# Kernel optimization log

Measured on AMD Instinct MI355X. Metric: run time of the kernel, lower is better.

The kernel has to match this reference:

```python
import jax, jax.numpy as jnp
import numpy as np

B, S, D = 2, 2048, 2560
H, HD = 32, 80           # n_head, head_dim = n_embd // n_head
RD = 32                  # rotary_dim (partial rotary, phi-style)
ROPE_BASE = 10000.0


def _rope_cache(seqlen, rotary_dim):
    # inv_freq = 1 / base^(2i/d); freqs = outer(t, inv_freq)  -> [S, RD//2]
    inv_freq = 1.0 / (ROPE_BASE ** (jnp.arange(0, rotary_dim, 2, dtype=jnp.float32) / rotary_dim))
    t = jnp.arange(seqlen, dtype=jnp.float32)
    freqs = jnp.outer(t, inv_freq)
    return jnp.cos(freqs), jnp.sin(freqs)


def setup_inputs() -> dict:
    key = jax.random.key(0)
    k0, k1, k2, k3, k4 = jax.random.split(key, 5)
    x = jax.random.normal(k0, (B, S, D), dtype=jnp.float32)
    wqkv_w = jax.random.normal(k1, (3 * D, D), dtype=jnp.float32) * 0.02
    wqkv_b = jax.random.normal(k2, (3 * D,), dtype=jnp.float32) * 0.02
    out_w = jax.random.normal(k3, (D, D), dtype=jnp.float32) * 0.02
    out_b = jax.random.normal(k4, (D,), dtype=jnp.float32) * 0.02
    return {"x": x, "wqkv_w": wqkv_w, "wqkv_b": wqkv_b, "out_w": out_w, "out_b": out_b}


def _attention_core(x, wqkv_w, wqkv_b, out_w, out_b):
    b, s, d = x.shape
    qkv = (x @ wqkv_w.T + wqkv_b).reshape(b, s, 3, H, HD)  # [B,S,3,H,HD]

    cos, sin = _rope_cache(s, RD)            # [S, RD//2]
    c = cos[:, None, :]                       # [S,1,RD//2]
    si = sin[:, None, :]

    def rot(t):  # partial NeoX-style rotary on first RD dims; t: [B,S,H,HD]
        t_rot, t_pass = t[..., :RD], t[..., RD:]
        t1, t2 = t_rot[..., : RD // 2], t_rot[..., RD // 2 :]
        return jnp.concatenate([t1 * c - t2 * si, t1 * si + t2 * c, t_pass], axis=-1)

    q = rot(qkv[:, :, 0])                     # [B,S,H,HD]
    k = rot(qkv[:, :, 1])
    v = qkv[:, :, 2]

    # fp32 scores = q @ (k * scale)^T, causal mask filled with -10000.0 (as in source)
    scale = 1.0 / np.sqrt(HD).astype(np.float32)
    scores = jnp.einsum("bqhd,bkhd->bhqk", q, k * scale)  # [B,H,S,S]
    causal_mask = jnp.arange(s)[None, :] > jnp.arange(s)[:, None]  # cols > rows
    scores = jnp.where(causal_mask, jnp.float32(-10000.0), scores)
    attn = jax.nn.softmax(scores, axis=-1)
    ctx = jnp.einsum("bhqk,bkhd->bqhd", attn, v).reshape(b, s, d)
    return ctx @ out_w.T + out_b


def reference(x, wqkv_w, wqkv_b, out_w, out_b):
    return _attention_core(x, wqkv_w, wqkv_b, out_w, out_b)
```

## Files before the change

### kernel.cpp

```cpp
#include <hip/hip_runtime.h>
#include <cstdint>
#include <cstddef>

#define B_  2
#define S_  2048
#define D_  2560
#define H_  32
#define HD_ 80

typedef __attribute__((ext_vector_type(8))) short  short8;
typedef __attribute__((ext_vector_type(4))) float  floatx4;

__device__ __forceinline__ float b2f(unsigned short u) {
  union { unsigned int i; float f; } x; x.i = ((unsigned int)u) << 16; return x.f;
}
__device__ __forceinline__ unsigned short f2bf(float f) {
  union { float f; unsigned int i; } x; x.f = f;
  unsigned int u = x.i;
  return (unsigned short)((u + 0x7fffu + ((u >> 16) & 1u)) >> 16);
}

__global__ void cvt3_kernel(const float* __restrict__ s0, unsigned short* __restrict__ d0, int n0,
                            const float* __restrict__ s1, unsigned short* __restrict__ d1, int n1,
                            const float* __restrict__ s2, unsigned short* __restrict__ d2, int n2) {
  int j = blockIdx.x * 256 + threadIdx.x;
  const float* s; unsigned short* d;
  if (j < n0) { s = s0; d = d0; }
  else {
    j -= n0;
    if (j < n1) { s = s1; d = d1; }
    else { j -= n1; if (j >= n2) return; s = s2; d = d2; }
  }
  const float4 v = ((const float4*)s)[j];
  ushort4 r;
  r.x = f2bf(v.x); r.y = f2bf(v.y); r.z = f2bf(v.z); r.w = f2bf(v.w);
  ((ushort4*)d)[j] = r;
}

#define GLOAD_LDS16(g, l)                                                      \
  __builtin_amdgcn_global_load_lds(                                            \
      (const __attribute__((address_space(1))) void*)(g),                      \
      (__attribute__((address_space(3))) void*)(l), 16, 0, 0)

template <int OUT_BF16>
__global__ __launch_bounds__(512)
void gemm256(const unsigned short* __restrict__ A,
             const unsigned short* __restrict__ Bw,
             const float* __restrict__ bias,
             void* __restrict__ Cv,
             const int M, const int N, const int K) {
  __shared__ __align__(16) unsigned short sh[65536];
  const int tid  = threadIdx.x;
  const int wave = tid >> 6;
  const int lane = tid & 63;
  const int wm = wave >> 2;
  const int wn = wave & 3;
  const int fr = lane & 15;
  const int fg = lane >> 4;
  const int row0 = (int)blockIdx.y << 8;
  const int col0 = (int)blockIdx.x << 8;
  const unsigned short* Ab = A  + (size_t)row0 * K;
  const unsigned short* Bb = Bw + (size_t)col0 * K;
  const int srow = lane >> 2;
  const int scol = ((lane & 3) << 3) ^ ((lane & 32) ? 16 : 0);
  const int rdoff = fr * 32 + ((fg * 8) ^ ((fr & 8) ? 16 : 0));
  const int aOff = wm * 8192;
  const int bOff = 16384 + (wn >> 1) * 8192;
  const int rbB  = (wn & 1) * 4;
  const int NT = K >> 6;

  floatx4 acc[8][4] = {};

#define STAGE_HALF(G, matOff, c, h, k0)                                        \
  do {                                                                         \
    _Pragma("unroll")                                                          \
    for (int i_ = 0; i_ < 2; ++i_) {                                           \
      const int s_ = (wave << 1) | i_;                                         \
      const int kk_ = s_ >> 3, rb_ = s_ & 7;                                   \
      GLOAD_LDS16((G) + (size_t)((h) * 128 + rb_ * 16 + srow) * K              \
                      + ((k0) + kk_ * 32 + scol),                              \
                  &sh[(c) * 32768 + (matOff) + (h) * 8192 + s_ * 512]);        \
    }                                                                          \
  } while (0)

  STAGE_HALF(Ab, 0,     0, 0, 0);
  STAGE_HALF(Ab, 0,     0, 1, 0);
  STAGE_HALF(Bb, 16384, 0, 0, 0);
  STAGE_HALF(Bb, 16384, 0, 1, 0);
  if (NT > 1) { STAGE_HALF(Ab, 0, 1, 0, 64); STAGE_HALF(Ab, 0, 1, 1, 64); }
  if (NT > 1) asm volatile("s_waitcnt vmcnt(4)" ::: "memory");
  else        asm volatile("s_waitcnt vmcnt(0)" ::: "memory");
  __builtin_amdgcn_s_barrier();

  for (int t = 0; t < NT; ++t) {
    const int c  = t & 1;
    const int cb = c << 15;
    short8 aF[4][2], bF0[2][2], bF1[2][2];
#pragma unroll
    for (int nj = 0; nj < 2; ++nj)
#pragma unroll
      for (int kk = 0; kk < 2; ++kk)
        bF0[nj][kk] = *(const short8*)&sh[cb + bOff + (kk * 8 + rbB + nj) * 512 + rdoff];
#pragma unroll
    for (int mi = 0; mi < 4; ++mi)
#pragma unroll
      for (int kk = 0; kk < 2; ++kk)
        aF[mi][kk] = *(const short8*)&sh[cb + aOff + (kk * 8 + mi) * 512 + rdoff];
    if (t + 1 < NT) STAGE_HALF(Bb, 16384, c ^ 1, 0, (t + 1) << 6);
    __builtin_amdgcn_s_barrier();
    __builtin_amdgcn_s_setprio(1);
#pragma unroll
    for (int kk = 0; kk < 2; ++kk)
#pragma unroll
      for (int mi = 0; mi < 4; ++mi)
#pragma unroll
        for (int nj = 0; nj < 2; ++nj)
          acc[mi][nj] = __builtin_amdgcn_mfma_f32_16x16x32_bf16(aF[mi][kk], bF0[nj][kk], acc[mi][nj], 0, 0, 0);
    __builtin_amdgcn_s_setprio(0);
    __builtin_amdgcn_s_barrier();
#pragma unroll
    for (int nj = 0; nj < 2; ++nj)
#pragma unroll
      for (int kk = 0; kk < 2; ++kk)
        bF1[nj][kk] = *(const short8*)&sh[cb + bOff + (kk * 8 + rbB + 2 + nj) * 512 + rdoff];
    if (t + 1 < NT) STAGE_HALF(Bb, 16384, c ^ 1, 1, (t + 1) << 6);
    __builtin_amdgcn_s_barrier();
    __builtin_amdgcn_s_setprio(1);
#pragma unroll
    for (int kk = 0; kk < 2; ++kk)
#pragma unroll
      for (int mi = 0; mi < 4; ++mi)
#pragma unroll
        for (int nj = 0; nj < 2; ++nj)
          acc[mi][2 + nj] = __builtin_amdgcn_mfma_f32_16x16x32_bf16(aF[mi][kk], bF1[nj][kk], acc[mi][2 + nj], 0, 0, 0);
    __builtin_amdgcn_s_setprio(0);
    __builtin_amdgcn_s_barrier();
#pragma unroll
    for (int mi = 0; mi < 4; ++mi)
#pragma unroll
      for (int kk = 0; kk < 2; ++kk)
        aF[mi][kk] = *(const short8*)&sh[cb + aOff + (kk * 8 + 4 + mi) * 512 + rdoff];
    __builtin_amdgcn_s_barrier();
    __builtin_amdgcn_s_setprio(1);
#pragma unroll
    for (int kk = 0; kk < 2; ++kk)
#pragma unroll
      for (int mi = 0; mi < 4; ++mi)
#pragma unroll
        for (int nj = 0; nj < 2; ++nj)
          acc[4 + mi][2 + nj] = __builtin_amdgcn_mfma_f32_16x16x32_bf16(aF[mi][kk], bF1[nj][kk], acc[4 + mi][2 + nj], 0, 0, 0);
    __builtin_amdgcn_s_setprio(0);
    __builtin_amdgcn_s_barrier();
    if (t + 2 < NT) {
      STAGE_HALF(Ab, 0, c, 0, (t + 2) << 6);
      STAGE_HALF(Ab, 0, c, 1, (t + 2) << 6);
    }
    __builtin_amdgcn_s_barrier();
    __builtin_amdgcn_s_setprio(1);
#pragma unroll
    for (int kk = 0; kk < 2; ++kk)
#pragma unroll
      for (int mi = 0; mi < 4; ++mi)
#pragma unroll
        for (int nj = 0; nj < 2; ++nj)
          acc[4 + mi][nj] = __builtin_amdgcn_mfma_f32_16x16x32_bf16(aF[mi][kk], bF0[nj][kk], acc[4 + mi][nj], 0, 0, 0);
    __builtin_amdgcn_s_setprio(0);
    if (t + 2 < NT)      asm volatile("s_waitcnt vmcnt(4)" ::: "memory");
    else if (t + 1 < NT) asm volatile("s_waitcnt vmcnt(0)" ::: "memory");
    __builtin_amdgcn_s_barrier();
  }
#undef STAGE_HALF

  unsigned short* Cb = (unsigned short*)Cv;
  float* Cf = (float*)Cv;
#pragma unroll
  for (int nj = 0; nj < 4; ++nj) {
    const int col = col0 + wn * 64 + nj * 16 + fr;
    const float bv = bias[col];
#pragma unroll
    for (int mi = 0; mi < 8; ++mi) {
      const int rowb = row0 + wm * 128 + mi * 16 + fg * 4;
#pragma unroll
      for (int r = 0; r < 4; ++r) {
        const float v = acc[mi][nj][r] + bv;
        const size_t idx = (size_t)(rowb + r) * N + col;
        if (OUT_BF16) Cb[idx] = f2bf(v);
        else          Cf[idx] = v;
      }
    }
  }
}

__global__ void rope_kernel(const unsigned short* __restrict__ qkv,
                            unsigned short* __restrict__ Q,
                            unsigned short* __restrict__ K) {
  const int idx = blockIdx.x * 256 + threadIdx.x;
  if (idx >= B_ * S_ * H_) return;
  const int h = idx & (H_ - 1);
  const int s = (idx >> 5) & (S_ - 1);
  const int b = idx >> 16;
  const unsigned short* row = qkv + (size_t)(b * S_ + s) * (3 * D_);
  const size_t obase = ((size_t)(b * H_ + h) * S_ + s) * HD_;

  float cc[16], ssn[16];
#pragma unroll
  for (int i = 0; i < 16; i++) {
    const float ang = (float)s * exp2f((float)i * -0.83048202372184059f);
    ssn[i] = sinf(ang);
    cc[i]  = cosf(ang);
  }
  {
    const float QS = 0.11180339887498949f * 1.4426950408889634f;
    const uint4* src = (const uint4*)(row + h * HD_);
    float f[80], g[80];
#pragma unroll
    for (int i = 0; i < 10; i++) {
      uint4 t = src[i];
      const unsigned short* w = (const unsigned short*)&t;
#pragma unroll
      for (int j = 0; j < 8; j++) f[i * 8 + j] = b2f(w[j]);
    }
#pragma unroll
    for (int i = 0; i < 16; i++) {
      g[i]      = f[i] * cc[i] - f[i + 16] * ssn[i];
      g[i + 16] = f[i] * ssn[i] + f[i + 16] * cc[i];
    }
#pragma unroll
    for (int i = 32; i < 80; i++) g[i] = f[i];
    uint4* dst = (uint4*)(Q + obase);
#pragma unroll
    for (int i = 0; i < 10; i++) {
      uint4 t;
      unsigned short* w = (unsigned short*)&t;
#pragma unroll
      for (int j = 0; j < 8; j++) w[j] = f2bf(g[i * 8 + j] * QS);
      dst[i] = t;
    }
  }
  {
    const uint4* src = (const uint4*)(row + (H_ + h) * HD_);
    float f[32], g[32];
#pragma unroll
    for (int i = 0; i < 4; i++) {
      uint4 t = src[i];
      const unsigned short* w = (const unsigned short*)&t;
#pragma unroll
      for (int j = 0; j < 8; j++) f[i * 8 + j] = b2f(w[j]);
    }
#pragma unroll
    for (int i = 0; i < 16; i++) {
      g[i]      = f[i] * cc[i] - f[i + 16] * ssn[i];
      g[i + 16] = f[i] * ssn[i] + f[i + 16] * cc[i];
    }
    uint4* dst = (uint4*)(K + obase);
#pragma unroll
    for (int i = 0; i < 4; i++) {
      uint4 t;
      unsigned short* w = (unsigned short*)&t;
#pragma unroll
      for (int j = 0; j < 8; j++) w[j] = f2bf(g[i * 8 + j]);
      dst[i] = t;
    }
#pragma unroll
    for (int i = 4; i < 10; i++) dst[i] = src[i];
  }
}

__global__ __launch_bounds__(256)
void vtrans_kernel(const unsigned short* __restrict__ qkv, unsigned short* __restrict__ Vt) {
  __shared__ unsigned short T[64][88];
  const int tid = threadIdx.x;
  const int bh = blockIdx.y;
  const int b = bh >> 5, h = bh & 31;
  const int tile = blockIdx.x;
  const int s0 = tile * 64;
  for (int t = tid; t < 640; t += 256) {
    const int r = t / 10, c = t % 10;
    const size_t src = ((size_t)((b * S_ + s0 + r) * 3) + 2) * D_ + h * HD_ + c * 8;
    *(uint4*)&T[r][c * 8] = *(const uint4*)&qkv[src];
  }
  __syncthreads();
  unsigned short* tb = Vt + ((size_t)bh * 32 + tile) * 5120;
  for (int t = tid; t < 640; t += 256) {
    const int d = t / 8, sc = t % 8;
    uint4 o;
    unsigned short* w = (unsigned short*)&o;
#pragma unroll
    for (int j = 0; j < 8; j++) w[j] = T[sc * 8 + j][d];
    *(uint4*)&tb[d * 64 + ((sc * 8) ^ ((d & 7) * 8))] = o;
  }
}

__global__ __launch_bounds__(256, 4)
void attn_mfma(const unsigned short* __restrict__ Qg,
               const unsigned short* __restrict__ Kg,
               const unsigned short* __restrict__ Vtg,
               unsigned short* __restrict__ ctx) {
  __shared__ unsigned short Ks[64 * 80];
  __shared__ unsigned short Vs[80 * 64];
  __shared__ unsigned short Ts[4][32 * 40];

  const int tid  = threadIdx.x;
  const int wave = tid >> 6;
  const int lane = tid & 63;
  const int fr   = lane & 15;
  const int fg   = lane >> 4;
  const int bh   = blockIdx.y;
  const int qt   = (int)gridDim.x - 1 - (int)blockIdx.x;
  const int qbase = (qt << 7) + wave * 32;

  const unsigned short* Qrow  = Qg  + (size_t)bh * S_ * HD_;
  const unsigned short* Krow  = Kg  + (size_t)bh * S_ * HD_;
  const unsigned short* Vtile = Vtg + (size_t)bh * 32 * 5120;

  short8 qf[2][3];
  const short8 zfrag = {};
#pragma unroll
  for (int mi = 0; mi < 2; mi++) {
    const unsigned short* qp = Qrow + (size_t)(qbase + mi * 16 + fr) * HD_;
    qf[mi][0] = *(const short8*)&qp[fg * 8];
    qf[mi][1] = *(const short8*)&qp[32 + fg * 8];
    qf[mi][2] = (fg < 2) ? *(const short8*)&qp[64 + fg * 8] : zfrag;
  }

  floatx4 accOT[5][2] = {};
  float l_part[2] = {0.f, 0.f};

  const int nch = 2 * qt + 2;
  for (int c = 0; c < nch; c++) {
    const int k0 = c * 64;
    __syncthreads();
    {
      const unsigned short* Kt = Krow + (size_t)k0 * HD_;
      for (int i = wave; i < 10; i += 4)
        GLOAD_LDS16(Kt + i * 512 + lane * 8, &Ks[i * 512]);
    }
    {
      const unsigned short* Vt = Vtile + (size_t)c * 5120;
      for (int i = wave; i < 10; i += 4)
        GLOAD_LDS16(Vt + i * 512 + lane * 8, &Vs[i * 512]);
    }
    __syncthreads();

    floatx4 accST[4][2] = {};
#pragma unroll
    for (int ni = 0; ni < 4; ni++) {
      const unsigned short* kp = &Ks[(ni * 16 + fr) * 80];
      const short8 kf0 = *(const short8*)&kp[fg * 8];
      const short8 kf1 = *(const short8*)&kp[32 + fg * 8];
      const short8 kf2 = *(const short8*)&kp[64 + (fg & 1) * 8];
      accST[ni][0] = __builtin_amdgcn_mfma_f32_16x16x32_bf16(kf0, qf[0][0], accST[ni][0], 0, 0, 0);
      accST[ni][1] = __builtin_amdgcn_mfma_f32_16x16x32_bf16(kf0, qf[1][0], accST[ni][1], 0, 0, 0);
      accST[ni][0] = __builtin_amdgcn_mfma_f32_16x16x32_bf16(kf1, qf[0][1], accST[ni][0], 0, 0, 0);
      accST[ni][1] = __builtin_amdgcn_mfma_f32_16x16x32_bf16(kf1, qf[1][1], accST[ni][1], 0, 0, 0);
      accST[ni][0] = __builtin_amdgcn_mfma_f32_16x16x32_bf16(kf2, qf[0][2], accST[ni][0], 0, 0, 0);
      accST[ni][1] = __builtin_amdgcn_mfma_f32_16x16x32_bf16(kf2, qf[1][2], accST[ni][1], 0, 0, 0);
    }

    if (k0 + 63 > qbase) {
#pragma unroll
      for (int ni = 0; ni < 4; ni++)
#pragma unroll
        for (int mi = 0; mi < 2; mi++) {
          const int qg = qbase + mi * 16 + fr;
#pragma unroll
          for (int r = 0; r < 4; r++) {
            const int kg = k0 + ni * 16 + fg * 4 + r;
            if (kg > qg) accST[ni][mi][r] = -1e30f;
          }
        }
    }

#pragma unroll
    for (int hh = 0; hh < 2; hh++) {
#pragma unroll
      for (int nh = 0; nh < 2; nh++) {
        const int ni = hh * 2 + nh;
#pragma unroll
        for (int mi = 0; mi < 2; mi++) {
          const float p0 = __builtin_amdgcn_exp2f(accST[ni][mi][0]);
          const float p1 = __builtin_amdgcn_exp2f(accST[ni][mi][1]);
          const float p2 = __builtin_amdgcn_exp2f(accST[ni][mi][2]);
          const float p3 = __builtin_amdgcn_exp2f(accST[ni][mi][3]);
          l_part[mi] += (p0 + p1) + (p2 + p3);
          uint2 w;
          w.x = (unsigned)f2bf(p0) | ((unsigned)f2bf(p1) << 16);
          w.y = (unsigned)f2bf(p2) | ((unsigned)f2bf(p3) << 16);
          *(uint2*)&Ts[wave][(mi * 16 + fr) * 40 + nh * 16 + fg * 4] = w;
        }
      }
      const short8 pf0 = *(const short8*)&Ts[wave][fr * 40 + fg * 8];
      const short8 pf1 = *(const short8*)&Ts[wave][(16 + fr) * 40 + fg * 8];
      const int vcol = hh * 32 + fg * 8;
#pragma unroll
      for (int dt = 0; dt < 5; dt++) {
        const short8 vf = *(const short8*)&Vs[(dt * 16 + fr) * 64 + (vcol ^ ((fr & 7) * 8))];
        accOT[dt][0] = __builtin_amdgcn_mfma_f32_16x16x32_bf16(vf, pf0, accOT[dt][0], 0, 0, 0);
        accOT[dt][1] = __builtin_amdgcn_mfma_f32_16x16x32_bf16(vf, pf1, accOT[dt][1], 0, 0, 0);
      }
    }
  }

  const int b = bh >> 5, h2 = bh & 31;
#pragma unroll
  for (int mi = 0; mi < 2; mi++) {
    float s = l_part[mi];
    s += __shfl_xor(s, 16);
    s += __shfl_xor(s, 32);
    const float inv = 1.f / s;
    const size_t rowoff = (size_t)(b * S_ + qbase + mi * 16 + fr) * D_ + h2 * HD_;
#pragma unroll
    for (int dt = 0; dt < 5; dt++) {
      const float v0 = accOT[dt][mi][0] * inv;
      const float v1 = accOT[dt][mi][1] * inv;
      const float v2 = accOT[dt][mi][2] * inv;
      const float v3 = accOT[dt][mi][3] * inv;
      uint2 w;
      w.x = (unsigned)f2bf(v0) | ((unsigned)f2bf(v1) << 16);
      w.y = (unsigned)f2bf(v2) | ((unsigned)f2bf(v3) << 16);
      *(uint2*)&ctx[rowoff + dt * 16 + fg * 4] = w;
    }
  }
}

extern "C" void kernel_launch(void* const* d_in, const int* in_sizes, int n_in,
                              void* d_out, int out_size, void* d_ws, size_t ws_size,
                              hipStream_t stream) {
  (void)in_sizes; (void)n_in; (void)out_size; (void)ws_size;
  const float* x      = (const float*)d_in[0];
  const float* wqkv_w = (const float*)d_in[1];
  const float* wqkv_b = (const float*)d_in[2];
  const float* out_w  = (const float*)d_in[3];
  const float* out_b  = (const float*)d_in[4];
  char* ws = (char*)d_ws;

  unsigned short* Xb    = (unsigned short*)(ws + 0);
  unsigned short* Wqkvb = (unsigned short*)(ws + 20971520);
  unsigned short* qkv   = (unsigned short*)(ws + 60293120);
  unsigned short* Qb    = (unsigned short*)(ws + 123207680);
  unsigned short* Kb    = (unsigned short*)(ws + 144179200);
  unsigned short* Woutb = (unsigned short*)(ws + 165150720);
  unsigned short* ctx   = Xb;
  unsigned short* Vtile = (unsigned short*)(ws + 34078720);

  cvt3_kernel<<<35840, 256, 0, stream>>>(x, Xb, 2621440,
                                         wqkv_w, Wqkvb, 4915200,
                                         out_w, Woutb, 1638400);
  gemm256<1><<<dim3(30, 16), 512, 0, stream>>>(Xb, Wqkvb, wqkv_b, (void*)qkv, 4096, 7680, 2560);
  rope_kernel<<<512, 256, 0, stream>>>(qkv, Qb, Kb);
  vtrans_kernel<<<dim3(32, 64), 256, 0, stream>>>(qkv, Vtile);
  attn_mfma<<<dim3(16, 64), 256, 0, stream>>>(Qb, Kb, Vtile, ctx);
  gemm256<0><<<dim3(10, 16), 512, 0, stream>>>(ctx, Woutb, out_b, d_out, 4096, 2560, 2560);
}
```

Measured before the change: 601.2 us.

## Cut barriers in GEMM main loop by hoisting fragment loads into fewer phases

Restructures the GEMM K-loop so both B sub-fragments and the low A fragments are read from LDS up front, and both B halves of the next tile are staged at once. The high A fragments load between MFMA groups. This drops the per-iteration workgroup barriers from about seven to two, and the final barrier is skipped on the last iteration. It costs extra registers for the separate A fragment sets and depends on the remaining barriers still protecting the double buffers from races.

```diff
diff --git a/kernel.cpp b/kernel.cpp
--- a/kernel.cpp
+++ b/kernel.cpp
@@ -95,7 +95,7 @@
   for (int t = 0; t < NT; ++t) {
     const int c  = t & 1;
     const int cb = c << 15;
-    short8 aF[4][2], bF0[2][2], bF1[2][2];
+    short8 aL[4][2], aH[4][2], bF0[2][2], bF1[2][2];
 #pragma unroll
     for (int nj = 0; nj < 2; ++nj)
 #pragma unroll
@@ -105,9 +105,16 @@
     for (int mi = 0; mi < 4; ++mi)
 #pragma unroll
       for (int kk = 0; kk < 2; ++kk)
-        aF[mi][kk] = *(const short8*)&sh[cb + aOff + (kk * 8 + mi) * 512 + rdoff];
-    if (t + 1 < NT) STAGE_HALF(Bb, 16384, c ^ 1, 0, (t + 1) << 6);
-    __builtin_amdgcn_s_barrier();
+        aL[mi][kk] = *(const short8*)&sh[cb + aOff + (kk * 8 + mi) * 512 + rdoff];
+#pragma unroll
+    for (int nj = 0; nj < 2; ++nj)
+#pragma unroll
+      for (int kk = 0; kk < 2; ++kk)
+        bF1[nj][kk] = *(const short8*)&sh[cb + bOff + (kk * 8 + rbB + 2 + nj) * 512 + rdoff];
+    if (t + 1 < NT) {
+      STAGE_HALF(Bb, 16384, c ^ 1, 0, (t + 1) << 6);
+      STAGE_HALF(Bb, 16384, c ^ 1, 1, (t + 1) << 6);
+    }
     __builtin_amdgcn_s_setprio(1);
 #pragma unroll
     for (int kk = 0; kk < 2; ++kk)
@@ -115,47 +122,35 @@
       for (int mi = 0; mi < 4; ++mi)
 #pragma unroll
         for (int nj = 0; nj < 2; ++nj)
-          acc[mi][nj] = __builtin_amdgcn_mfma_f32_16x16x32_bf16(aF[mi][kk], bF0[nj][kk], acc[mi][nj], 0, 0, 0);
+          acc[mi][nj] = __builtin_amdgcn_mfma_f32_16x16x32_bf16(aL[mi][kk], bF0[nj][kk], acc[mi][nj], 0, 0, 0);
+    __builtin_amdgcn_s_setprio(0);
+#pragma unroll
+    for (int mi = 0; mi < 4; ++mi)
+#pragma unroll
+      for (int kk = 0; kk < 2; ++kk)
+        aH[mi][kk] = *(const short8*)&sh[cb + aOff + (kk * 8 + 4 + mi) * 512 + rdoff];
+    __builtin_amdgcn_s_setprio(1);
+#pragma unroll
+    for (int kk = 0; kk < 2; ++kk)
+#pragma unroll
+      for (int mi = 0; mi < 4; ++mi)
+#pragma unroll
+        for (int nj = 0; nj < 2; ++nj)
+          acc[mi][2 + nj] = __builtin_amdgcn_mfma_f32_16x16x32_bf16(aL[mi][kk], bF1[nj][kk], acc[mi][2 + nj], 0, 0, 0);
+#pragma unroll
+    for (int kk = 0; kk < 2; ++kk)
+#pragma unroll
+      for (int mi = 0; mi < 4; ++mi)
+#pragma unroll
+        for (int nj = 0; nj < 2; ++nj)
+          acc[4 + mi][2 + nj] = __builtin_amdgcn_mfma_f32_16x16x32_bf16(aH[mi][kk], bF1[nj][kk], acc[4 + mi][2 + nj], 0, 0, 0);
     __builtin_amdgcn_s_setprio(0);
     __builtin_amdgcn_s_barrier();
-#pragma unroll
-    for (int nj = 0; nj < 2; ++nj)
-#pragma unroll
-      for (int kk = 0; kk < 2; ++kk)
-        bF1[nj][kk] = *(const short8*)&sh[cb + bOff + (kk * 8 + rbB + 2 + nj) * 512 + rdoff];
-    if (t + 1 < NT) STAGE_HALF(Bb, 16384, c ^ 1, 1, (t + 1) << 6);
-    __builtin_amdgcn_s_barrier();
-    __builtin_amdgcn_s_setprio(1);
-#pragma unroll
-    for (int kk = 0; kk < 2; ++kk)
-#pragma unroll
-      for (int mi = 0; mi < 4; ++mi)
-#pragma unroll
-        for (int nj = 0; nj < 2; ++nj)
-          acc[mi][2 + nj] = __builtin_amdgcn_mfma_f32_16x16x32_bf16(aF[mi][kk], bF1[nj][kk], acc[mi][2 + nj], 0, 0, 0);
-    __builtin_amdgcn_s_setprio(0);
-    __builtin_amdgcn_s_barrier();
-#pragma unroll
-    for (int mi = 0; mi < 4; ++mi)
-#pragma unroll
-      for (int kk = 0; kk < 2; ++kk)
-        aF[mi][kk] = *(const short8*)&sh[cb + aOff + (kk * 8 + 4 + mi) * 512 + rdoff];
-    __builtin_amdgcn_s_barrier();
-    __builtin_amdgcn_s_setprio(1);
-#pragma unroll
-    for (int kk = 0; kk < 2; ++kk)
-#pragma unroll
-      for (int mi = 0; mi < 4; ++mi)
-#pragma unroll
-        for (int nj = 0; nj < 2; ++nj)
-          acc[4 + mi][2 + nj] = __builtin_amdgcn_mfma_f32_16x16x32_bf16(aF[mi][kk], bF1[nj][kk], acc[4 + mi][2 + nj], 0, 0, 0);
-    __builtin_amdgcn_s_setprio(0);
-    __builtin_amdgcn_s_barrier();
+    __builtin_amdgcn_sched_barrier(0);
     if (t + 2 < NT) {
       STAGE_HALF(Ab, 0, c, 0, (t + 2) << 6);
       STAGE_HALF(Ab, 0, c, 1, (t + 2) << 6);
     }
-    __builtin_amdgcn_s_barrier();
     __builtin_amdgcn_s_setprio(1);
 #pragma unroll
     for (int kk = 0; kk < 2; ++kk)
@@ -163,11 +158,11 @@
       for (int mi = 0; mi < 4; ++mi)
 #pragma unroll
         for (int nj = 0; nj < 2; ++nj)
-          acc[4 + mi][nj] = __builtin_amdgcn_mfma_f32_16x16x32_bf16(aF[mi][kk], bF0[nj][kk], acc[4 + mi][nj], 0, 0, 0);
+          acc[4 + mi][nj] = __builtin_amdgcn_mfma_f32_16x16x32_bf16(aH[mi][kk], bF0[nj][kk], acc[4 + mi][nj], 0, 0, 0);
     __builtin_amdgcn_s_setprio(0);
     if (t + 2 < NT)      asm volatile("s_waitcnt vmcnt(4)" ::: "memory");
     else if (t + 1 < NT) asm volatile("s_waitcnt vmcnt(0)" ::: "memory");
-    __builtin_amdgcn_s_barrier();
+    if (t + 1 < NT) __builtin_amdgcn_s_barrier();
   }
 #undef STAGE_HALF
 
```

Measured after the change: 568.4 us. 1.06x faster.
